# Kernel tuning notes

Measured on AMD Instinct MI355X. Metric: run time of the kernel, lower is better.

## Reference

```python
import jax, jax.numpy as jnp
import numpy as np

F, E, B = 30, 16, 4096
IN = F * E          # 480 = sum of embed dims
H1, H2 = 1024, 512  # fcn_dims
K = 32              # low-rank adapter k
HH = 512            # hyper hidden dim
D = 3               # domain_num
V = 10000           # vocab per field
EPS = 1e-5


def _bn(h, g, b):
    # BatchNorm1d in training mode: biased batch stats
    mu = h.mean(0)
    var = h.var(0)
    return g * (h - mu) * jax.lax.rsqrt(var + EPS) + b


def setup_inputs() -> dict:
    key = jax.random.key(0)
    ks = jax.random.split(key, 10)
    x = jax.random.randint(ks[0], (F, B), 0, V)
    # last row of x is the domain id, must be in [0, D)
    x = x.at[-1].set(jax.random.randint(ks[1], (B,), 0, D))
    w = lambda k_, s: jax.random.normal(k_, s, jnp.float32) * 0.02
    return {
        "x": x,
        "emb_tables": w(ks[2], (F, V, E)),
        # per-domain MLP (stacked over D): Linear/BN x2 + final Linear(H2->1)
        "dW0": w(ks[3], (D, IN, H1)), "db0": jnp.zeros((D, H1)),
        "dg0": jnp.ones((D, H1)), "dbt0": jnp.zeros((D, H1)),
        "dW1": w(ks[4], (D, H1, H2)), "db1": jnp.zeros((D, H2)),
        "dg1": jnp.ones((D, H2)), "dbt1": jnp.zeros((D, H2)),
        "dWo": w(ks[5], (D, H2, 1)), "dbo": jnp.zeros((D, 1)),
        # hyper_net: Linear+BN+ReLU (IN->HH), Linear+BN+ReLU (HH->K*K)
        "hW0": w(ks[6], (IN, HH)), "hb0": jnp.zeros((HH,)),
        "hg0": jnp.ones((HH,)), "hbt0": jnp.zeros((HH,)),
        "hW1": w(ks[7], (HH, K * K)), "hb1": jnp.zeros((K * K,)),
        "hg1": jnp.ones((K * K,)), "hbt1": jnp.zeros((K * K,)),
        # low-rank factors (torch inits these to ones)
        "u0": jnp.ones((H2, K)), "u1": jnp.ones((32, K)),
        "v0": jnp.ones((K, 32)), "v1": jnp.ones((K, H2)),
        "bl0": jnp.zeros((32,)), "bl1": jnp.zeros((H2,)),
        "gamma1": jnp.ones((H2,)), "bias1": jnp.zeros((H2,)),
    }


def reference(x, emb_tables, dW0, db0, dg0, dbt0, dW1, db1, dg1, dbt1,
              dWo, dbo, hW0, hb0, hg0, hbt0, hW1, hb1, hg1, hbt1,
              u0, u1, v0, v1, bl0, bl1, gamma1, bias1):
    domain_id = x[-1]                                        # [B]
    emb = jax.vmap(lambda t, idx: t[idx])(emb_tables, x)     # [F, B, E]
    emb = emb.transpose(1, 0, 2).reshape(x.shape[1], -1)     # [B, F*E]

    # hyper-net output is identical across the domain loop -> compute once
    h = jax.nn.relu(_bn(emb @ hW0 + hb0, hg0, hbt0))
    h = jax.nn.relu(_bn(h @ hW1 + hb1, hg1, hbt1))
    hyper = h.reshape(-1, K, K)                              # [B, K, K]
    w1 = jnp.einsum('mi,bij,jn->bmn', u0, hyper, v0)         # [B, H2, 32]
    w2 = jnp.einsum('mi,bij,jn->bmn', u1, hyper, v1)         # [B, 32, H2]

    outs = []
    for d in range(D):
        di = jax.nn.relu(_bn(emb @ dW0[d] + db0[d], dg0[d], dbt0[d]))  # [B, H1]
        di = jax.nn.relu(_bn(di @ dW1[d] + db1[d], dg1[d], dbt1[d]))   # [B, H2]
        t = jax.nn.sigmoid(jnp.einsum('bf,bfj->bj', di, w1) + bl0)     # [B, 32]
        t = jnp.einsum('bf,bfj->bj', t, w2) + bl1                      # [B, H2]
        # manual batch-norm with torch.var (unbiased, ddof=1)
        mean, var = t.mean(0), t.var(0, ddof=1)
        out = gamma1 * (t - mean) / jnp.sqrt(var + EPS) + bias1
        di = out + di                                                  # residual
        outs.append(jax.nn.sigmoid(di @ dWo[d] + dbo[d]))              # [B, 1]

    final = jnp.zeros_like(outs[0])
    for d in range(D):
        final = jnp.where((domain_id == d)[:, None], outs[d], final)
    return final
```

## Files before the change

### kernel.cpp

```cpp
#include <hip/hip_runtime.h>
#include <hip/hip_bf16.h>
#include <math.h>

#define F_   30
#define E_   16
#define B_   4096
#define IN_  480
#define H1_  1024
#define H2_  512
#define K_   32
#define HH_  512
#define D_   3
#define V_   10000
#define EPS_ 1e-5f

typedef __attribute__((ext_vector_type(8))) short bf16x8;
typedef __attribute__((ext_vector_type(4))) float f32x4;
typedef __attribute__((ext_vector_type(8))) unsigned short u16x8;

__device__ __forceinline__ unsigned short f2bf(float f) {
    unsigned u = __builtin_bit_cast(unsigned, f);
    u += 0x7FFFu + ((u >> 16) & 1u);
    return (unsigned short)(u >> 16);
}
__device__ __forceinline__ float bf2f(unsigned short h) {
    return __builtin_bit_cast(float, ((unsigned)h) << 16);
}
__device__ __forceinline__ void gload_lds16(const unsigned short* g, unsigned short* l) {
    typedef unsigned int __attribute__((address_space(1))) guint;
    typedef unsigned int __attribute__((address_space(3))) luint;
    __builtin_amdgcn_global_load_lds((const guint*)g, (luint*)l, 16, 0, 0);
}

__global__ __launch_bounds__(256) void gather_kernel(const int* __restrict__ x,
                                                     const float* __restrict__ tables,
                                                     unsigned short* __restrict__ emb) {
    int idx = blockIdx.x * 256 + threadIdx.x;
    int b = idx / (F_ * 2);
    int r = idx - b * (F_ * 2);
    int f = r >> 1, h = r & 1;
    int row = x[f * B_ + b];
    const float4* src = reinterpret_cast<const float4*>(tables + ((size_t)f * V_ + row) * E_ + h * 8);
    float4 v0 = src[0], v1 = src[1];
    u16x8 o;
    o[0]=f2bf(v0.x); o[1]=f2bf(v0.y); o[2]=f2bf(v0.z); o[3]=f2bf(v0.w);
    o[4]=f2bf(v1.x); o[5]=f2bf(v1.y); o[6]=f2bf(v1.z); o[7]=f2bf(v1.w);
    *reinterpret_cast<u16x8*>(emb + (size_t)b * IN_ + f * E_ + h * 8) = o;
}

struct TransArgs {
    const float* src[9];
    unsigned short* dst[9];
    int K[9], N[9], base[9];
};
__global__ __launch_bounds__(256) void transpose_bf16_kernel(TransArgs ta) {
    __shared__ float tile[32][33];
    int blk = blockIdx.x;
    int seg = 0;
#pragma unroll
    for (int i = 1; i < 9; i++) if (blk >= ta.base[i]) seg = i;
    int tix = blk - ta.base[seg];
    int Kd = ta.K[seg], Nd = ta.N[seg];
    int tn = Nd >> 5;
    int k0 = (tix / tn) << 5;
    int n0 = (tix - (tix / tn) * tn) << 5;
    const float* src = ta.src[seg];
    unsigned short* dst = ta.dst[seg];
    int t = threadIdx.x;
    int c = t & 31, rr = t >> 5;
#pragma unroll
    for (int i = 0; i < 4; i++) {
        int r = rr + i * 8;
        tile[r][c] = src[(size_t)(k0 + r) * Nd + n0 + c];
    }
    __syncthreads();
#pragma unroll
    for (int i = 0; i < 4; i++) {
        int r = rr + i * 8;
        dst[(size_t)(n0 + r) * Kd + k0 + c] = f2bf(tile[c][r]);
    }
}

__global__ __launch_bounds__(256) void convert_bf16_kernel(const float* __restrict__ s,
                                                           unsigned short* __restrict__ d, int n) {
    int i = blockIdx.x * 256 + threadIdx.x;
    if (i < n) d[i] = f2bf(s[i]);
}

struct GemmGroups {
    const unsigned short* A[4];
    const unsigned short* Bt[4];
    void* C[4];
    float* stats[4];
    int N[4], K[4], base[4], obf[4];
};
__global__ __launch_bounds__(256) void gemm_grouped(GemmGroups p) {
    __shared__ unsigned short sA[128 * 32];
    __shared__ unsigned short sB[128 * 32];
    int blk = blockIdx.x;
    int g = 0;
#pragma unroll
    for (int i = 1; i < 4; i++) if (blk >= p.base[i]) g = i;
    int tix = blk - p.base[g];
    int N = p.N[g], K = p.K[g];
    const unsigned short* A = p.A[g];
    const unsigned short* Bt = p.Bt[g];
    float* stats = p.stats[g];
    int bm = (tix & 31) << 7;
    int bn = (tix >> 5) << 7;

    int tid = threadIdx.x;
    int l = tid & 63, w = tid >> 6;
    int wr = w >> 1, wc = w & 1;
    const unsigned short* Ab = A + (size_t)bm * K;
    const unsigned short* Bb = Bt + (size_t)bn * K;
    f32x4 acc[4][4] = {};
    int n0c = tid, n1c = tid + 256;
    int r0 = n0c >> 2, lc0 = (n0c & 3) ^ ((r0 >> 1) & 3);
    int r1 = n1c >> 2, lc1 = (n1c & 3) ^ ((r1 >> 1) & 3);
    int kg = l >> 4, lr = l & 15;
    for (int k0 = 0; k0 < K; k0 += 32) {
        gload_lds16(Ab + (size_t)r0 * K + k0 + lc0 * 8, &sA[n0c * 8]);
        gload_lds16(Ab + (size_t)r1 * K + k0 + lc1 * 8, &sA[n1c * 8]);
        gload_lds16(Bb + (size_t)r0 * K + k0 + lc0 * 8, &sB[n0c * 8]);
        gload_lds16(Bb + (size_t)r1 * K + k0 + lc1 * 8, &sB[n1c * 8]);
        __syncthreads();
        bf16x8 af[4], bfr[4];
#pragma unroll
        for (int m = 0; m < 4; m++) {
            int R = (wr << 6) + (m << 4) + lr;
            af[m] = *reinterpret_cast<const bf16x8*>(&sA[R * 32 + ((kg ^ ((R >> 1) & 3)) << 3)]);
        }
#pragma unroll
        for (int n = 0; n < 4; n++) {
            int R = (wc << 6) + (n << 4) + lr;
            bfr[n] = *reinterpret_cast<const bf16x8*>(&sB[R * 32 + ((kg ^ ((R >> 1) & 3)) << 3)]);
        }
#pragma unroll
        for (int m = 0; m < 4; m++)
#pragma unroll
            for (int n = 0; n < 4; n++)
                acc[m][n] = __builtin_amdgcn_mfma_f32_16x16x32_bf16(af[m], bfr[n], acc[m][n], 0, 0, 0);
        __syncthreads();
    }
    int orow = bm + (wr << 6) + (kg << 2);
    int ocol = bn + (wc << 6) + lr;
    if (p.obf[g]) {
        unsigned short* Cb = (unsigned short*)p.C[g];
#pragma unroll
        for (int m = 0; m < 4; m++)
#pragma unroll
            for (int n = 0; n < 4; n++)
#pragma unroll
                for (int j = 0; j < 4; j++)
                    Cb[(size_t)(orow + (m << 4) + j) * N + ocol + (n << 4)] = f2bf(acc[m][n][j]);
    } else {
        float* C = (float*)p.C[g];
#pragma unroll
        for (int m = 0; m < 4; m++)
#pragma unroll
            for (int n = 0; n < 4; n++)
#pragma unroll
                for (int j = 0; j < 4; j++)
                    C[(size_t)(orow + (m << 4) + j) * N + ocol + (n << 4)] = acc[m][n][j];
    }
#pragma unroll
    for (int n = 0; n < 4; n++) {
        float s = 0.f, ss = 0.f;
#pragma unroll
        for (int m = 0; m < 4; m++)
#pragma unroll
            for (int j = 0; j < 4; j++) {
                float v = acc[m][n][j];
                s += v; ss += v * v;
            }
        s  += __shfl_xor(s, 16);  s  += __shfl_xor(s, 32);
        ss += __shfl_xor(ss, 16); ss += __shfl_xor(ss, 32);
        if (l < 16) {
            int col = bn + (wc << 6) + (n << 4) + lr;
            atomicAdd(&stats[col], s);
            atomicAdd(&stats[N + col], ss);
        }
    }
}

__global__ __launch_bounds__(256) void gemm_bf16_N32(const unsigned short* __restrict__ D1BF,
                                                     const unsigned short* __restrict__ Bt,
                                                     float* __restrict__ Afac) {
    __shared__ unsigned short sA[128 * 32];
    __shared__ unsigned short sB[32 * 32];
    int d = blockIdx.y;
    const unsigned short* A = D1BF + (size_t)d * B_ * H2_;
    float* C = Afac + (size_t)d * B_ * 32;
    const int K = 512;
    int tid = threadIdx.x;
    int l = tid & 63, w = tid >> 6;
    int bm = blockIdx.x << 7;
    const unsigned short* Ab = A + (size_t)bm * K;
    f32x4 acc[2][2] = {};
    int n0c = tid, n1c = tid + 256;
    int r0 = n0c >> 2, lc0 = (n0c & 3) ^ ((r0 >> 1) & 3);
    int r1 = n1c >> 2, lc1 = (n1c & 3) ^ ((r1 >> 1) & 3);
    int kg = l >> 4, lr = l & 15;
    for (int k0 = 0; k0 < K; k0 += 32) {
        gload_lds16(Ab + (size_t)r0 * K + k0 + lc0 * 8, &sA[n0c * 8]);
        gload_lds16(Ab + (size_t)r1 * K + k0 + lc1 * 8, &sA[n1c * 8]);
        if (tid < 128)
            gload_lds16(Bt + (size_t)r0 * K + k0 + lc0 * 8, &sB[n0c * 8]);
        __syncthreads();
        bf16x8 af[2], bfr[2];
#pragma unroll
        for (int m = 0; m < 2; m++) {
            int R = (w << 5) + (m << 4) + lr;
            af[m] = *reinterpret_cast<const bf16x8*>(&sA[R * 32 + ((kg ^ ((R >> 1) & 3)) << 3)]);
        }
#pragma unroll
        for (int n = 0; n < 2; n++) {
            int R = (n << 4) + lr;
            bfr[n] = *reinterpret_cast<const bf16x8*>(&sB[R * 32 + ((kg ^ ((R >> 1) & 3)) << 3)]);
        }
#pragma unroll
        for (int m = 0; m < 2; m++)
#pragma unroll
            for (int n = 0; n < 2; n++)
                acc[m][n] = __builtin_amdgcn_mfma_f32_16x16x32_bf16(af[m], bfr[n], acc[m][n], 0, 0, 0);
        __syncthreads();
    }
    int orow = bm + (w << 5) + (kg << 2);
#pragma unroll
    for (int m = 0; m < 2; m++)
#pragma unroll
        for (int n = 0; n < 2; n++)
#pragma unroll
            for (int j = 0; j < 4; j++)
                C[(size_t)(orow + (m << 4) + j) * 32 + (n << 4) + lr] = acc[m][n][j];
}

__global__ __launch_bounds__(256) void bn480_kernel(const unsigned short* __restrict__ Z480bf,
                                                    const float* __restrict__ stats,
                                                    const float* __restrict__ hg0,
                                                    const float* __restrict__ hbt0,
                                                    const float* __restrict__ dg0,
                                                    const float* __restrict__ dbt0,
                                                    unsigned short* __restrict__ Z0BF,
                                                    unsigned short* __restrict__ ZD0BF) {
    int idx = blockIdx.x * 256 + threadIdx.x;
    int b = idx / 448;
    int c0 = (idx - b * 448) * 8;
    const float* g;
    const float* bt;
    unsigned short* dst;
    if (c0 < 512) {
        g = hg0 + c0; bt = hbt0 + c0;
        dst = Z0BF + (size_t)b * 512 + c0;
    } else {
        int d = (c0 - 512) >> 10, cc = (c0 - 512) & 1023;
        g = dg0 + d * 1024 + cc; bt = dbt0 + d * 1024 + cc;
        dst = ZD0BF + ((size_t)d << 22) + (size_t)b * 1024 + cc;
    }
    u16x8 v = *reinterpret_cast<const u16x8*>(Z480bf + (size_t)b * 3584 + c0);
    u16x8 o;
#pragma unroll
    for (int q = 0; q < 8; q++) {
        float S = stats[c0 + q], SS = stats[3584 + c0 + q];
        float m = S * (1.f / B_);
        float var = (SS - S * m) * (1.f / B_);
        float rs = rsqrtf(var + EPS_);
        o[q] = f2bf(fmaxf(0.f, g[q] * (bf2f(v[q]) - m) * rs + bt[q]));
    }
    *reinterpret_cast<u16x8*>(dst) = o;
}

__global__ __launch_bounds__(256) void bn_l1_kernel(const float* __restrict__ Z1scr,
                                                    const float* __restrict__ SCR1,
                                                    const float* __restrict__ statsH,
                                                    const float* __restrict__ statsD1,
                                                    const float* __restrict__ hg1,
                                                    const float* __restrict__ hbt1,
                                                    const float* __restrict__ dg1,
                                                    const float* __restrict__ dbt1,
                                                    unsigned short* __restrict__ Hbf,
                                                    unsigned short* __restrict__ D1BF) {
    int gidx = blockIdx.x * 256 + threadIdx.x;
    const float* Z; const float* stats; const float* g; const float* bt;
    unsigned short* outp; int c0; int idx;
    if (gidx < 524288) {
        idx = gidx;
        c0 = (idx & 127) * 8;
        Z = Z1scr; stats = statsH; g = hg1; bt = hbt1; outp = Hbf;
    } else {
        idx = gidx - 524288;
        int row = idx >> 6;
        int d = row >> 12;
        c0 = (idx & 63) * 8;
        Z = SCR1; stats = statsD1 + d * 1024; g = dg1 + d * 512; bt = dbt1 + d * 512; outp = D1BF;
    }
    int sh = (gidx < 524288) ? 1024 : 512;
    float4 v0 = reinterpret_cast<const float4*>(Z)[(size_t)idx * 2];
    float4 v1 = reinterpret_cast<const float4*>(Z)[(size_t)idx * 2 + 1];
    float r[8] = {v0.x, v0.y, v0.z, v0.w, v1.x, v1.y, v1.z, v1.w};
    u16x8 o;
#pragma unroll
    for (int q = 0; q < 8; q++) {
        float S = stats[c0 + q], SS = stats[sh + c0 + q];
        float m = S * (1.f / B_);
        float var = (SS - S * m) * (1.f / B_);
        float rs = rsqrtf(var + EPS_);
        o[q] = f2bf(fmaxf(0.f, g[c0 + q] * (r[q] - m) * rs + bt[c0 + q]));
    }
    *reinterpret_cast<u16x8*>(outp + (size_t)idx * 8) = o;
}

__global__ __launch_bounds__(256) void adapter_core(const float* __restrict__ Afac,
                                                    const unsigned short* __restrict__ Hbf,
                                                    const float* __restrict__ v0,
                                                    const float* __restrict__ u1,
                                                    const float* __restrict__ bl0,
                                                    float* __restrict__ C2) {
    __shared__ float sv0[K_ * K_];
    __shared__ float su1[K_ * K_];
    int t = threadIdx.x;
    reinterpret_cast<float4*>(sv0)[t] = reinterpret_cast<const float4*>(v0)[t];
    reinterpret_cast<float4*>(su1)[t] = reinterpret_cast<const float4*>(u1)[t];
    __syncthreads();
    int w = t >> 6, l = t & 63;
    int i = l & 31;
    int b = blockIdx.x * 4 + w;
    float hreg[32];
#pragma unroll
    for (int k = 0; k < 32; k++) hreg[k] = bf2f(Hbf[(size_t)b * 1024 + k * 32 + i]);
    float bl0i = bl0[i];
#pragma unroll
    for (int d = 0; d < 3; d++) {
        float a = Afac[(size_t)d * 131072 + b * 32 + i];
        float c = 0.f;
#pragma unroll
        for (int k = 0; k < 32; k++) c += __shfl(a, k) * hreg[k];
        float targ = bl0i;
#pragma unroll
        for (int k = 0; k < 32; k++) targ += __shfl(c, k) * sv0[k * 32 + i];
        float tv = 1.f / (1.f + expf(-targ));
        float a2 = 0.f;
#pragma unroll
        for (int k = 0; k < 32; k++) a2 += __shfl(tv, k) * su1[k * 32 + i];
        float c2 = 0.f;
#pragma unroll
        for (int k = 0; k < 32; k++) c2 += __shfl(a2, k) * hreg[k];
        if (l < 32) C2[(size_t)d * 131072 + b * 32 + i] = c2;
    }
}

__global__ __launch_bounds__(256) void t2_expand(const float* __restrict__ C2,
                                                 const unsigned short* __restrict__ v1bf,
                                                 float* __restrict__ T2) {
    __shared__ unsigned short sv1[K_ * H2_];
    int t = threadIdx.x;
#pragma unroll
    for (int i2 = 0; i2 < 8; i2++)
        *reinterpret_cast<u16x8*>(&sv1[(i2 * 256 + t) * 8]) =
            *reinterpret_cast<const u16x8*>(&v1bf[(i2 * 256 + t) * 8]);
    __syncthreads();
    int w = t >> 6, l = t & 63;
    int idx = blockIdx.x * 4 + w;
    float cv = C2[(size_t)idx * 32 + (l & 31)];
    float o[8] = {};
#pragma unroll
    for (int k = 0; k < 32; k++) {
        float cb = __shfl(cv, k);
        u16x8 vv = *reinterpret_cast<const u16x8*>(&sv1[k * 512 + l * 8]);
#pragma unroll
        for (int q = 0; q < 8; q++) o[q] += cb * bf2f(vv[q]);
    }
    float4* dst = reinterpret_cast<float4*>(&T2[(size_t)idx * 512 + l * 8]);
    dst[0] = make_float4(o[0], o[1], o[2], o[3]);
    dst[1] = make_float4(o[4], o[5], o[6], o[7]);
}

__global__ __launch_bounds__(256) void colpartialT2(const float* __restrict__ T2,
                                                    float* __restrict__ statsT2) {
    int z = blockIdx.z;
    const float* Z = T2 + (size_t)z * 2097152;
    float* colsum = statsT2 + z * 1024;
    float* colsumsq = colsum + 512;
    int lc = threadIdx.x & 63;
    int c  = blockIdx.x * 64 + lc;
    int rg = threadIdx.x >> 6;
    int r0 = blockIdx.y * 128 + rg;
    float s = 0.f, ss = 0.f;
#pragma unroll 8
    for (int k = 0; k < 32; k++) {
        float v = Z[(size_t)(r0 + 4 * k) * 512 + c];
        s += v; ss += v * v;
    }
    __shared__ float sh[2][4][64];
    sh[0][rg][lc] = s;
    sh[1][rg][lc] = ss;
    __syncthreads();
    if (threadIdx.x < 64) {
        int cc = blockIdx.x * 64 + threadIdx.x;
        float S  = sh[0][0][threadIdx.x] + sh[0][1][threadIdx.x] + sh[0][2][threadIdx.x] + sh[0][3][threadIdx.x];
        float SS = sh[1][0][threadIdx.x] + sh[1][1][threadIdx.x] + sh[1][2][threadIdx.x] + sh[1][3][threadIdx.x];
        atomicAdd(&colsum[cc], S);
        atomicAdd(&colsumsq[cc], SS);
    }
}

__global__ __launch_bounds__(256) void head_kernel(const int* __restrict__ x,
                                                   const float* __restrict__ T2,
                                                   const unsigned short* __restrict__ D1BF,
                                                   const float* __restrict__ statsT2,
                                                   const float* __restrict__ g1,
                                                   const float* __restrict__ b1,
                                                   const float* __restrict__ dWo,
                                                   const float* __restrict__ dbo,
                                                   float* __restrict__ out) {
    int b = blockIdx.x, t = threadIdx.x;
    int d = x[(F_ - 1) * B_ + b];
    const float* T2d = T2 + (size_t)d * 2097152;
    const unsigned short* D1d = D1BF + (size_t)d * 2097152;
    const float* colsum = statsT2 + d * 1024;
    const float* colsumsq = colsum + 512;
    const float* wo = dWo + d * 512;
    float p = 0.f;
#pragma unroll
    for (int q = 0; q < 2; q++) {
        int j = t + q * 256;
        float S = colsum[j], SS = colsumsq[j];
        float m = S * (1.f / B_);
        float var = (SS - S * m) * (1.f / (B_ - 1));
        float rs = rsqrtf(var + EPS_);
        float di = g1[j] * (T2d[(size_t)b * H2_ + j] - m) * rs + b1[j] + bf2f(D1d[(size_t)b * H2_ + j]);
        p += di * wo[j];
    }
    p += __shfl_down(p, 32); p += __shfl_down(p, 16); p += __shfl_down(p, 8);
    p += __shfl_down(p, 4);  p += __shfl_down(p, 2);  p += __shfl_down(p, 1);
    __shared__ float sw[4];
    if ((t & 63) == 0) sw[t >> 6] = p;
    __syncthreads();
    if (t == 0) {
        float logit = sw[0] + sw[1] + sw[2] + sw[3] + dbo[d];
        out[b] = 1.f / (1.f + expf(-logit));
    }
}

__global__ __launch_bounds__(256) void zero_kernel(float* __restrict__ p, int n) {
    int i = blockIdx.x * 256 + threadIdx.x;
    if (i < n) p[i] = 0.f;
}

extern "C" void kernel_launch(void* const* d_in, const int* in_sizes, int n_in,
                              void* d_out, int out_size, void* d_ws, size_t ws_size,
                              hipStream_t stream) {
    const int*   x      = (const int*)  d_in[0];
    const float* tables = (const float*)d_in[1];
    const float* dW0  = (const float*)d_in[2];
    const float* dg0  = (const float*)d_in[4];
    const float* dbt0 = (const float*)d_in[5];
    const float* dW1  = (const float*)d_in[6];
    const float* dg1  = (const float*)d_in[8];
    const float* dbt1 = (const float*)d_in[9];
    const float* dWo  = (const float*)d_in[10];
    const float* dbo  = (const float*)d_in[11];
    const float* hW0  = (const float*)d_in[12];
    const float* hg0  = (const float*)d_in[14];
    const float* hbt0 = (const float*)d_in[15];
    const float* hW1  = (const float*)d_in[16];
    const float* hg1  = (const float*)d_in[18];
    const float* hbt1 = (const float*)d_in[19];
    const float* u0   = (const float*)d_in[20];
    const float* u1   = (const float*)d_in[21];
    const float* v0   = (const float*)d_in[22];
    const float* v1   = (const float*)d_in[23];
    const float* bl0  = (const float*)d_in[24];
    const float* g1   = (const float*)d_in[26];
    const float* b1   = (const float*)d_in[27];
    float* out = (float*)d_out;

    float* ws       = (float*)d_ws;
    float* stats480 = ws;
    float* statsH   = stats480 + 7168;
    float* statsD1  = statsH + 2048;
    float* statsT2  = statsD1 + 3072;
    float* Afac     = statsT2 + 3072;
    float* C2       = Afac + 393216;
    float* Z1scr    = C2 + 393216;
    float* SCR1     = Z1scr + 4194304;
    float* T2       = SCR1 + 6291456;
    unsigned short* Z480bf = (unsigned short*)(T2 + 6291456);
    unsigned short* embBF = Z480bf + 14680064;
    unsigned short* Z0BF  = embBF + 1966080;
    unsigned short* ZD0BF = Z0BF + 2097152;
    unsigned short* Hbf   = ZD0BF + 12582912;
    unsigned short* D1BF  = Hbf + 4194304;
    unsigned short* W480  = D1BF + 6291456;
    unsigned short* hW1t  = W480 + 1720320;
    unsigned short* dW1t  = hW1t + 524288;
    unsigned short* u0t   = dW1t + 1572864;
    unsigned short* v1bf  = u0t + 16384;

    zero_kernel<<<60, 256, 0, stream>>>(ws, 15360);
    gather_kernel<<<960, 256, 0, stream>>>(x, tables, embBF);

    TransArgs ta;
    ta.src[0] = hW0; ta.dst[0] = W480; ta.K[0] = 480; ta.N[0] = 512;
    ta.src[1] = hW1; ta.dst[1] = hW1t; ta.K[1] = 512; ta.N[1] = 1024;
    for (int d = 0; d < 3; d++) {
        ta.src[2 + d] = dW0 + (size_t)d * 480 * 1024;
        ta.dst[2 + d] = W480 + (size_t)(512 + d * 1024) * 480;
        ta.K[2 + d] = 480; ta.N[2 + d] = 1024;
        ta.src[5 + d] = dW1 + (size_t)d * 1024 * 512;
        ta.dst[5 + d] = dW1t + (size_t)d * 512 * 1024;
        ta.K[5 + d] = 1024; ta.N[5 + d] = 512;
    }
    ta.src[8] = u0; ta.dst[8] = u0t; ta.K[8] = 512; ta.N[8] = 32;
    int acc_t = 0;
    for (int i = 0; i < 9; i++) { ta.base[i] = acc_t; acc_t += (ta.K[i] >> 5) * (ta.N[i] >> 5); }
    transpose_bf16_kernel<<<acc_t, 256, 0, stream>>>(ta);
    convert_bf16_kernel<<<64, 256, 0, stream>>>(v1, v1bf, 16384);

    GemmGroups g480;
    g480.A[0] = embBF; g480.Bt[0] = W480; g480.C[0] = Z480bf;
    g480.stats[0] = stats480; g480.N[0] = 3584; g480.K[0] = 480; g480.base[0] = 0; g480.obf[0] = 1;
    for (int i = 1; i < 4; i++) { g480.base[i] = 0x7fffffff; g480.A[i] = nullptr; g480.Bt[i] = nullptr; g480.C[i] = nullptr; g480.stats[i] = nullptr; g480.N[i] = 0; g480.K[i] = 32; g480.obf[i] = 0; }
    gemm_grouped<<<896, 256, 0, stream>>>(g480);
    bn480_kernel<<<7168, 256, 0, stream>>>(Z480bf, stats480, hg0, hbt0, dg0, dbt0, Z0BF, ZD0BF);

    GemmGroups g2;
    g2.A[0] = Z0BF; g2.Bt[0] = hW1t; g2.C[0] = Z1scr;
    g2.stats[0] = statsH; g2.N[0] = 1024; g2.K[0] = 512; g2.base[0] = 0; g2.obf[0] = 0;
    for (int d = 0; d < 3; d++) {
        g2.A[1 + d] = ZD0BF + (size_t)d * 4194304;
        g2.Bt[1 + d] = dW1t + (size_t)d * 524288;
        g2.C[1 + d] = SCR1 + (size_t)d * 2097152;
        g2.stats[1 + d] = statsD1 + d * 1024;
        g2.N[1 + d] = 512; g2.K[1 + d] = 1024;
        g2.base[1 + d] = 256 + d * 128;
        g2.obf[1 + d] = 0;
    }
    gemm_grouped<<<640, 256, 0, stream>>>(g2);
    bn_l1_kernel<<<5120, 256, 0, stream>>>(Z1scr, SCR1, statsH, statsD1, hg1, hbt1, dg1, dbt1, Hbf, D1BF);

    gemm_bf16_N32<<<dim3(32, 3), 256, 0, stream>>>(D1BF, u0t, Afac);
    adapter_core<<<1024, 256, 0, stream>>>(Afac, Hbf, v0, u1, bl0, C2);
    t2_expand<<<3072, 256, 0, stream>>>(C2, v1bf, T2);
    colpartialT2<<<dim3(8, 32, 3), 256, 0, stream>>>(T2, statsT2);
    head_kernel<<<4096, 256, 0, stream>>>(x, T2, D1BF, statsT2, g1, b1, dWo, dbo, out);
    (void)in_sizes; (void)n_in; (void)out_size; (void)ws_size;
}
```

Baseline: 287.0 us.

## Compute T2 batch stats via Gram matrix and recompute T2 in head

Stops materializing the per-domain T2 tensor (three 4096x512 fp32 buffers). The column sums and sums of squares are instead derived from a 32x32 Gram matrix of C2 and its column sums, projected through v1. The head kernel recomputes T2 only for the row's selected domain on the fly. It also merges the zero, gather, transpose and convert launches into one prep kernel. Together these remove large T2 writes and reads plus several launches. The trade-off is that sum-of-squares via the Gram form may lose some numerical precision.

```diff
diff --git a/kernel.cpp b/kernel.cpp
--- a/kernel.cpp
+++ b/kernel.cpp
@@ -32,59 +32,68 @@
     __builtin_amdgcn_global_load_lds((const guint*)g, (luint*)l, 16, 0, 0);
 }
 
-__global__ __launch_bounds__(256) void gather_kernel(const int* __restrict__ x,
-                                                     const float* __restrict__ tables,
-                                                     unsigned short* __restrict__ emb) {
-    int idx = blockIdx.x * 256 + threadIdx.x;
-    int b = idx / (F_ * 2);
-    int r = idx - b * (F_ * 2);
-    int f = r >> 1, h = r & 1;
-    int row = x[f * B_ + b];
-    const float4* src = reinterpret_cast<const float4*>(tables + ((size_t)f * V_ + row) * E_ + h * 8);
-    float4 v0 = src[0], v1 = src[1];
-    u16x8 o;
-    o[0]=f2bf(v0.x); o[1]=f2bf(v0.y); o[2]=f2bf(v0.z); o[3]=f2bf(v0.w);
-    o[4]=f2bf(v1.x); o[5]=f2bf(v1.y); o[6]=f2bf(v1.z); o[7]=f2bf(v1.w);
-    *reinterpret_cast<u16x8*>(emb + (size_t)b * IN_ + f * E_ + h * 8) = o;
-}
-
 struct TransArgs {
     const float* src[9];
     unsigned short* dst[9];
     int K[9], N[9], base[9];
 };
-__global__ __launch_bounds__(256) void transpose_bf16_kernel(TransArgs ta) {
+#define PREP_ZB   73
+#define PREP_GA   (PREP_ZB + 960)
+#define PREP_TR   (PREP_GA + 3744)
+#define PREP_CV   (PREP_TR + 64)
+__global__ __launch_bounds__(256) void prep_kernel(TransArgs ta,
+                                                   float* __restrict__ zero_p, int zero_n,
+                                                   const int* __restrict__ x,
+                                                   const float* __restrict__ tables,
+                                                   unsigned short* __restrict__ emb,
+                                                   const float* __restrict__ v1,
+                                                   unsigned short* __restrict__ v1bf) {
     __shared__ float tile[32][33];
     int blk = blockIdx.x;
-    int seg = 0;
-#pragma unroll
-    for (int i = 1; i < 9; i++) if (blk >= ta.base[i]) seg = i;
-    int tix = blk - ta.base[seg];
-    int Kd = ta.K[seg], Nd = ta.N[seg];
-    int tn = Nd >> 5;
-    int k0 = (tix / tn) << 5;
-    int n0 = (tix - (tix / tn) * tn) << 5;
-    const float* src = ta.src[seg];
-    unsigned short* dst = ta.dst[seg];
     int t = threadIdx.x;
-    int c = t & 31, rr = t >> 5;
-#pragma unroll
-    for (int i = 0; i < 4; i++) {
-        int r = rr + i * 8;
-        tile[r][c] = src[(size_t)(k0 + r) * Nd + n0 + c];
-    }
-    __syncthreads();
-#pragma unroll
-    for (int i = 0; i < 4; i++) {
-        int r = rr + i * 8;
-        dst[(size_t)(n0 + r) * Kd + k0 + c] = f2bf(tile[c][r]);
-    }
-}
-
-__global__ __launch_bounds__(256) void convert_bf16_kernel(const float* __restrict__ s,
-                                                           unsigned short* __restrict__ d, int n) {
-    int i = blockIdx.x * 256 + threadIdx.x;
-    if (i < n) d[i] = f2bf(s[i]);
+    if (blk < PREP_ZB) {
+        int i = blk * 256 + t;
+        if (i < zero_n) zero_p[i] = 0.f;
+    } else if (blk < PREP_GA) {
+        int idx = (blk - PREP_ZB) * 256 + t;
+        int b = idx / (F_ * 2);
+        int r = idx - b * (F_ * 2);
+        int f = r >> 1, h = r & 1;
+        int row = x[f * B_ + b];
+        const float4* src = reinterpret_cast<const float4*>(tables + ((size_t)f * V_ + row) * E_ + h * 8);
+        float4 v0 = src[0], v1v = src[1];
+        u16x8 o;
+        o[0]=f2bf(v0.x); o[1]=f2bf(v0.y); o[2]=f2bf(v0.z); o[3]=f2bf(v0.w);
+        o[4]=f2bf(v1v.x); o[5]=f2bf(v1v.y); o[6]=f2bf(v1v.z); o[7]=f2bf(v1v.w);
+        *reinterpret_cast<u16x8*>(emb + (size_t)b * IN_ + f * E_ + h * 8) = o;
+    } else if (blk < PREP_TR) {
+        int gblk = blk - PREP_GA;
+        int seg = 0;
+#pragma unroll
+        for (int i = 1; i < 9; i++) if (gblk >= ta.base[i]) seg = i;
+        int tix = gblk - ta.base[seg];
+        int Kd = ta.K[seg], Nd = ta.N[seg];
+        int tn = Nd >> 5;
+        int k0 = (tix / tn) << 5;
+        int n0 = (tix - (tix / tn) * tn) << 5;
+        const float* src = ta.src[seg];
+        unsigned short* dst = ta.dst[seg];
+        int c = t & 31, rr = t >> 5;
+#pragma unroll
+        for (int i = 0; i < 4; i++) {
+            int r = rr + i * 8;
+            tile[r][c] = src[(size_t)(k0 + r) * Nd + n0 + c];
+        }
+        __syncthreads();
+#pragma unroll
+        for (int i = 0; i < 4; i++) {
+            int r = rr + i * 8;
+            dst[(size_t)(n0 + r) * Kd + k0 + c] = f2bf(tile[c][r]);
+        }
+    } else {
+        int i = (blk - PREP_TR) * 256 + t;
+        if (i < K_ * H2_) v1bf[i] = f2bf(v1[i]);
+    }
 }
 
 struct GemmGroups {
@@ -350,102 +359,130 @@
     }
 }
 
-__global__ __launch_bounds__(256) void t2_expand(const float* __restrict__ C2,
-                                                 const unsigned short* __restrict__ v1bf,
-                                                 float* __restrict__ T2) {
+__global__ __launch_bounds__(256) void gram_kernel(const float* __restrict__ C2,
+                                                   float* __restrict__ gramM,
+                                                   float* __restrict__ gramS) {
+    __shared__ float sc[256 * 32];
+    int z = blockIdx.y;
+    const float* Cz = C2 + (size_t)z * 131072 + (size_t)blockIdx.x * 256 * 32;
+    int t = threadIdx.x;
+#pragma unroll
+    for (int i = 0; i < 8; i++)
+        reinterpret_cast<float4*>(sc)[t + i * 256] = reinterpret_cast<const float4*>(Cz)[t + i * 256];
+    __syncthreads();
+    int k = t >> 3, k4 = (t & 7) << 2;
+    float m0 = 0.f, m1 = 0.f, m2 = 0.f, m3 = 0.f;
+    for (int r = 0; r < 256; r++) {
+        float ck = sc[r * 32 + k];
+        m0 += ck * sc[r * 32 + k4 + 0];
+        m1 += ck * sc[r * 32 + k4 + 1];
+        m2 += ck * sc[r * 32 + k4 + 2];
+        m3 += ck * sc[r * 32 + k4 + 3];
+    }
+    float* Mz = gramM + z * 1024 + k * 32 + k4;
+    atomicAdd(&Mz[0], m0); atomicAdd(&Mz[1], m1);
+    atomicAdd(&Mz[2], m2); atomicAdd(&Mz[3], m3);
+    if (t < 32) {
+        float s = 0.f;
+        for (int r = 0; r < 256; r++) s += sc[r * 32 + t];
+        atomicAdd(&gramS[z * 32 + t], s);
+    }
+}
+
+__global__ __launch_bounds__(256) void stats_t2_kernel(const float* __restrict__ gramM,
+                                                       const float* __restrict__ gramS,
+                                                       const unsigned short* __restrict__ v1bf,
+                                                       float* __restrict__ statsT2) {
+    __shared__ float sM[1024];
+    __shared__ float sS[32];
     __shared__ unsigned short sv1[K_ * H2_];
+    int z = blockIdx.x;
     int t = threadIdx.x;
-#pragma unroll
-    for (int i2 = 0; i2 < 8; i2++)
-        *reinterpret_cast<u16x8*>(&sv1[(i2 * 256 + t) * 8]) =
-            *reinterpret_cast<const u16x8*>(&v1bf[(i2 * 256 + t) * 8]);
+    reinterpret_cast<float4*>(sM)[t] = reinterpret_cast<const float4*>(gramM + z * 1024)[t];
+    if (t < 8) reinterpret_cast<float4*>(sS)[t] = reinterpret_cast<const float4*>(gramS + z * 32)[t];
+#pragma unroll
+    for (int i = 0; i < 8; i++)
+        reinterpret_cast<u16x8*>(sv1)[t + i * 256] = reinterpret_cast<const u16x8*>(v1bf)[t + i * 256];
     __syncthreads();
-    int w = t >> 6, l = t & 63;
-    int idx = blockIdx.x * 4 + w;
-    float cv = C2[(size_t)idx * 32 + (l & 31)];
-    float o[8] = {};
-#pragma unroll
-    for (int k = 0; k < 32; k++) {
-        float cb = __shfl(cv, k);
-        u16x8 vv = *reinterpret_cast<const u16x8*>(&sv1[k * 512 + l * 8]);
-#pragma unroll
-        for (int q = 0; q < 8; q++) o[q] += cb * bf2f(vv[q]);
-    }
-    float4* dst = reinterpret_cast<float4*>(&T2[(size_t)idx * 512 + l * 8]);
-    dst[0] = make_float4(o[0], o[1], o[2], o[3]);
-    dst[1] = make_float4(o[4], o[5], o[6], o[7]);
-}
-
-__global__ __launch_bounds__(256) void colpartialT2(const float* __restrict__ T2,
-                                                    float* __restrict__ statsT2) {
-    int z = blockIdx.z;
-    const float* Z = T2 + (size_t)z * 2097152;
-    float* colsum = statsT2 + z * 1024;
-    float* colsumsq = colsum + 512;
-    int lc = threadIdx.x & 63;
-    int c  = blockIdx.x * 64 + lc;
-    int rg = threadIdx.x >> 6;
-    int r0 = blockIdx.y * 128 + rg;
-    float s = 0.f, ss = 0.f;
-#pragma unroll 8
-    for (int k = 0; k < 32; k++) {
-        float v = Z[(size_t)(r0 + 4 * k) * 512 + c];
-        s += v; ss += v * v;
-    }
-    __shared__ float sh[2][4][64];
-    sh[0][rg][lc] = s;
-    sh[1][rg][lc] = ss;
-    __syncthreads();
-    if (threadIdx.x < 64) {
-        int cc = blockIdx.x * 64 + threadIdx.x;
-        float S  = sh[0][0][threadIdx.x] + sh[0][1][threadIdx.x] + sh[0][2][threadIdx.x] + sh[0][3][threadIdx.x];
-        float SS = sh[1][0][threadIdx.x] + sh[1][1][threadIdx.x] + sh[1][2][threadIdx.x] + sh[1][3][threadIdx.x];
-        atomicAdd(&colsum[cc], S);
-        atomicAdd(&colsumsq[cc], SS);
+#pragma unroll
+    for (int jj = 0; jj < 2; jj++) {
+        int j = t + jj * 256;
+        float vj[32];
+#pragma unroll
+        for (int k = 0; k < 32; k++) vj[k] = bf2f(sv1[k * 512 + j]);
+        float cs = 0.f, ssq = 0.f;
+#pragma unroll
+        for (int k = 0; k < 32; k++) {
+            float wk = 0.f;
+#pragma unroll
+            for (int kp = 0; kp < 32; kp++) wk += sM[k * 32 + kp] * vj[kp];
+            ssq += vj[k] * wk;
+            cs += sS[k] * vj[k];
+        }
+        statsT2[z * 1024 + j] = cs;
+        statsT2[z * 1024 + 512 + j] = ssq;
     }
 }
 
 __global__ __launch_bounds__(256) void head_kernel(const int* __restrict__ x,
-                                                   const float* __restrict__ T2,
+                                                   const float* __restrict__ C2,
                                                    const unsigned short* __restrict__ D1BF,
                                                    const float* __restrict__ statsT2,
                                                    const float* __restrict__ g1,
                                                    const float* __restrict__ b1,
                                                    const float* __restrict__ dWo,
                                                    const float* __restrict__ dbo,
+                                                   const unsigned short* __restrict__ v1bf,
                                                    float* __restrict__ out) {
-    int b = blockIdx.x, t = threadIdx.x;
+    __shared__ unsigned short sv1[K_ * H2_];
+    int t = threadIdx.x;
+#pragma unroll
+    for (int i = 0; i < 8; i++)
+        reinterpret_cast<u16x8*>(sv1)[t + i * 256] = reinterpret_cast<const u16x8*>(v1bf)[t + i * 256];
+    __syncthreads();
+    int w = t >> 6, l = t & 63;
+    int b = blockIdx.x * 4 + w;
     int d = x[(F_ - 1) * B_ + b];
-    const float* T2d = T2 + (size_t)d * 2097152;
-    const unsigned short* D1d = D1BF + (size_t)d * 2097152;
-    const float* colsum = statsT2 + d * 1024;
-    const float* colsumsq = colsum + 512;
-    const float* wo = dWo + d * 512;
+    float cv = C2[((size_t)d * B_ + b) * 32 + (l & 31)];
+    float o[8] = {};
+#pragma unroll
+    for (int k = 0; k < 32; k++) {
+        float cb = __shfl(cv, k);
+        u16x8 vv = *reinterpret_cast<const u16x8*>(&sv1[k * 512 + l * 8]);
+#pragma unroll
+        for (int q = 0; q < 8; q++) o[q] += cb * bf2f(vv[q]);
+    }
+    int j0 = l * 8;
+    const float* cs = statsT2 + d * 1024;
+    float4 Sa = *reinterpret_cast<const float4*>(cs + j0);
+    float4 Sb = *reinterpret_cast<const float4*>(cs + j0 + 4);
+    float4 Qa = *reinterpret_cast<const float4*>(cs + 512 + j0);
+    float4 Qb = *reinterpret_cast<const float4*>(cs + 512 + j0 + 4);
+    float4 Ga = *reinterpret_cast<const float4*>(g1 + j0);
+    float4 Gb = *reinterpret_cast<const float4*>(g1 + j0 + 4);
+    float4 Ba = *reinterpret_cast<const float4*>(b1 + j0);
+    float4 Bb = *reinterpret_cast<const float4*>(b1 + j0 + 4);
+    float4 Wa = *reinterpret_cast<const float4*>(dWo + d * 512 + j0);
+    float4 Wb = *reinterpret_cast<const float4*>(dWo + d * 512 + j0 + 4);
+    u16x8 d1v = *reinterpret_cast<const u16x8*>(D1BF + (size_t)d * 2097152 + (size_t)b * 512 + j0);
+    float Sv[8] = {Sa.x,Sa.y,Sa.z,Sa.w,Sb.x,Sb.y,Sb.z,Sb.w};
+    float Qv[8] = {Qa.x,Qa.y,Qa.z,Qa.w,Qb.x,Qb.y,Qb.z,Qb.w};
+    float Gv[8] = {Ga.x,Ga.y,Ga.z,Ga.w,Gb.x,Gb.y,Gb.z,Gb.w};
+    float Bv[8] = {Ba.x,Ba.y,Ba.z,Ba.w,Bb.x,Bb.y,Bb.z,Bb.w};
+    float Wv[8] = {Wa.x,Wa.y,Wa.z,Wa.w,Wb.x,Wb.y,Wb.z,Wb.w};
     float p = 0.f;
 #pragma unroll
-    for (int q = 0; q < 2; q++) {
-        int j = t + q * 256;
-        float S = colsum[j], SS = colsumsq[j];
+    for (int q = 0; q < 8; q++) {
+        float S = Sv[q], SS = Qv[q];
         float m = S * (1.f / B_);
         float var = (SS - S * m) * (1.f / (B_ - 1));
         float rs = rsqrtf(var + EPS_);
-        float di = g1[j] * (T2d[(size_t)b * H2_ + j] - m) * rs + b1[j] + bf2f(D1d[(size_t)b * H2_ + j]);
-        p += di * wo[j];
+        float di = Gv[q] * (o[q] - m) * rs + Bv[q] + bf2f(d1v[q]);
+        p += di * Wv[q];
     }
     p += __shfl_down(p, 32); p += __shfl_down(p, 16); p += __shfl_down(p, 8);
     p += __shfl_down(p, 4);  p += __shfl_down(p, 2);  p += __shfl_down(p, 1);
-    __shared__ float sw[4];
-    if ((t & 63) == 0) sw[t >> 6] = p;
-    __syncthreads();
-    if (t == 0) {
-        float logit = sw[0] + sw[1] + sw[2] + sw[3] + dbo[d];
-        out[b] = 1.f / (1.f + expf(-logit));
-    }
-}
-
-__global__ __launch_bounds__(256) void zero_kernel(float* __restrict__ p, int n) {
-    int i = blockIdx.x * 256 + threadIdx.x;
-    if (i < n) p[i] = 0.f;
+    if (l == 0) out[b] = 1.f / (1.f + expf(-(p + dbo[d])));
 }
 
 extern "C" void kernel_launch(void* const* d_in, const int* in_sizes, int n_in,
@@ -481,12 +518,13 @@
     float* statsH   = stats480 + 7168;
     float* statsD1  = statsH + 2048;
     float* statsT2  = statsD1 + 3072;
-    float* Afac     = statsT2 + 3072;
+    float* gramM    = statsT2 + 3072;
+    float* gramS    = gramM + 3072;
+    float* Afac     = ws + 18560;
     float* C2       = Afac + 393216;
     float* Z1scr    = C2 + 393216;
     float* SCR1     = Z1scr + 4194304;
-    float* T2       = SCR1 + 6291456;
-    unsigned short* Z480bf = (unsigned short*)(T2 + 6291456);
+    unsigned short* Z480bf = (unsigned short*)(SCR1 + 6291456);
     unsigned short* embBF = Z480bf + 14680064;
     unsigned short* Z0BF  = embBF + 1966080;
     unsigned short* ZD0BF = Z0BF + 2097152;
@@ -498,9 +536,6 @@
     unsigned short* u0t   = dW1t + 1572864;
     unsigned short* v1bf  = u0t + 16384;
 
-    zero_kernel<<<60, 256, 0, stream>>>(ws, 15360);
-    gather_kernel<<<960, 256, 0, stream>>>(x, tables, embBF);
-
     TransArgs ta;
     ta.src[0] = hW0; ta.dst[0] = W480; ta.K[0] = 480; ta.N[0] = 512;
     ta.src[1] = hW1; ta.dst[1] = hW1t; ta.K[1] = 512; ta.N[1] = 1024;
@@ -515,8 +550,8 @@
     ta.src[8] = u0; ta.dst[8] = u0t; ta.K[8] = 512; ta.N[8] = 32;
     int acc_t = 0;
     for (int i = 0; i < 9; i++) { ta.base[i] = acc_t; acc_t += (ta.K[i] >> 5) * (ta.N[i] >> 5); }
-    transpose_bf16_kernel<<<acc_t, 256, 0, stream>>>(ta);
-    convert_bf16_kernel<<<64, 256, 0, stream>>>(v1, v1bf, 16384);
+
+    prep_kernel<<<PREP_CV, 256, 0, stream>>>(ta, ws, 18560, x, tables, embBF, v1, v1bf);
 
     GemmGroups g480;
     g480.A[0] = embBF; g480.Bt[0] = W480; g480.C[0] = Z480bf;
@@ -542,8 +577,8 @@
 
     gemm_bf16_N32<<<dim3(32, 3), 256, 0, stream>>>(D1BF, u0t, Afac);
     adapter_core<<<1024, 256, 0, stream>>>(Afac, Hbf, v0, u1, bl0, C2);
-    t2_expand<<<3072, 256, 0, stream>>>(C2, v1bf, T2);
-    colpartialT2<<<dim3(8, 32, 3), 256, 0, stream>>>(T2, statsT2);
-    head_kernel<<<4096, 256, 0, stream>>>(x, T2, D1BF, statsT2, g1, b1, dWo, dbo, out);
+    gram_kernel<<<dim3(16, 3), 256, 0, stream>>>(C2, gramM, gramS);
+    stats_t2_kernel<<<3, 256, 0, stream>>>(gramM, gramS, v1bf, statsT2);
+    head_kernel<<<1024, 256, 0, stream>>>(x, C2, D1BF, statsT2, g1, b1, dWo, dbo, v1bf, out);
     (void)in_sizes; (void)n_in; (void)out_size; (void)ws_size;
 }
```

Result: no change. 283.9 us (-1.1%).
